# Optimization experiments

Measured on AMD Instinct MI355X. Metric: run time of the kernel, lower is better.

## Reference

```python
import jax, jax.numpy as jnp
import numpy as np

HIDDEN = 2048
NUM_V = 16
NUM_K = 8
HK = 128
HV = 128
KCONV = 4
KEY_DIM = NUM_K * HK      # 1024
VALUE_DIM = NUM_V * HV    # 2048
CONV_DIM = 2 * KEY_DIM + VALUE_DIM  # 4096
R = NUM_V // NUM_K        # 2
L2_EPS = 1e-6
NORM_EPS = 1e-6


def setup_inputs() -> dict:
    key = jax.random.key(0)
    ks = jax.random.split(key, 8)
    s = 0.02
    return {
        "hidden_states": jax.random.normal(ks[0], (1, 1024, HIDDEN), jnp.float32),
        "w_qkvz": jax.random.normal(ks[1], (2 * KEY_DIM + 2 * VALUE_DIM, HIDDEN), jnp.float32) * s,
        "w_ba": jax.random.normal(ks[2], (2 * NUM_V, HIDDEN), jnp.float32) * s,
        "conv_w": jax.random.normal(ks[3], (CONV_DIM, KCONV), jnp.float32) * s,
        "dt_bias": jnp.ones((NUM_V,), jnp.float32),
        "A_log": jnp.log(jax.random.uniform(ks[4], (NUM_V,), jnp.float32, 1e-3, 16.0)),
        "norm_weight": jnp.ones((HV,), jnp.float32),
        "w_out": jax.random.normal(ks[5], (HIDDEN, VALUE_DIM), jnp.float32) * s,
    }


def reference(hidden_states, w_qkvz, w_ba, conv_w, dt_bias, A_log, norm_weight, w_out):
    B, T, _ = hidden_states.shape
    # --- input projections ---
    qkvz = hidden_states @ w_qkvz.T                     # [B,T,2K+2V]
    ba = hidden_states @ w_ba.T                         # [B,T,2*Hv]
    # fix_query_key_value_ordering: group by k-head, layout [hk, hk, r*hv, r*hv]
    qkvz = qkvz.reshape(B, T, NUM_K, 2 * HK + 2 * R * HV)
    q, k, v, z = jnp.split(qkvz, [HK, 2 * HK, 2 * HK + R * HV], axis=3)
    v = v.reshape(B, T, NUM_V, HV)
    z = z.reshape(B, T, NUM_V, HV)
    ba = ba.reshape(B, T, NUM_K, 2 * R)
    b = ba[..., :R].reshape(B, T, NUM_V)
    a = ba[..., R:].reshape(B, T, NUM_V)
    # --- depthwise causal conv1d + silu over concatenated q,k,v ---
    mixed = jnp.concatenate(
        [q.reshape(B, T, KEY_DIM), k.reshape(B, T, KEY_DIM), v.reshape(B, T, VALUE_DIM)], axis=-1
    )
    xc = mixed.transpose(0, 2, 1)                       # [B,C,T]
    yc = jax.lax.conv_general_dilated(
        xc, conv_w[:, None, :], (1,), [(KCONV - 1, 0)],
        feature_group_count=CONV_DIM, dimension_numbers=("NCH", "OIH", "NCH"),
    )
    yc = jax.nn.silu(yc).transpose(0, 2, 1)             # [B,T,C]
    q, k, v = jnp.split(yc, [KEY_DIM, 2 * KEY_DIM], axis=-1)
    q = q.reshape(B, T, NUM_K, HK)
    k = k.reshape(B, T, NUM_K, HK)
    v = v.reshape(B, T, NUM_V, HV)
    # --- gates ---
    beta = jax.nn.sigmoid(b)                            # [B,T,Hv]
    g = -jnp.exp(A_log) * jax.nn.softplus(a + dt_bias)  # [B,T,Hv] (log decay, <=0)
    # GQA expansion of q,k to value heads
    q = jnp.repeat(q, R, axis=2)                        # [B,T,Hv,hk]
    k = jnp.repeat(k, R, axis=2)
    # l2 norm on q,k (use_qk_l2norm_in_kernel=True)
    q = q * jax.lax.rsqrt(jnp.sum(q * q, -1, keepdims=True) + L2_EPS)
    k = k * jax.lax.rsqrt(jnp.sum(k * k, -1, keepdims=True) + L2_EPS)
    scale = HK ** -0.5
    # --- gated delta rule recurrence ---
    def step(S, xs):
        qt, kt, vt, gt, bt = xs                          # per-timestep slices
        S = S * jnp.exp(gt)[..., None, None]             # decay state [B,Hv,hk,hv]
        kv = jnp.einsum("bhk,bhkv->bhv", kt, S)          # readout at k_t
        delta = (vt - kv) * bt[..., None]                # beta-gated delta
        S = S + jnp.einsum("bhk,bhv->bhkv", kt, delta)
        o = jnp.einsum("bhk,bhkv->bhv", qt * scale, S)
        return S, o

    S0 = jnp.zeros((B, NUM_V, HK, HV), hidden_states.dtype)
    xs = (
        q.transpose(1, 0, 2, 3), k.transpose(1, 0, 2, 3), v.transpose(1, 0, 2, 3),
        g.transpose(1, 0, 2), beta.transpose(1, 0, 2),
    )
    _, o = jax.lax.scan(step, S0, xs)                   # o: [T,B,Hv,hv]
    o = o.transpose(1, 0, 2, 3)                         # [B,T,Hv,hv]
    # --- gated RMSNorm (gate applied before normalization, Mamba2/Qwen3Next style) ---
    xf = o.astype(jnp.float32) * jax.nn.silu(z.astype(jnp.float32))
    var = jnp.mean(xf * xf, -1, keepdims=True)
    xn = xf * jax.lax.rsqrt(var + NORM_EPS) * norm_weight
    # --- output projection ---
    return xn.reshape(B, T, VALUE_DIM) @ w_out.T
```

## Files before the change

kernel.cpp:

```cpp
#include <hip/hip_runtime.h>
#include <math.h>

#define T_LEN   1024
#define HIDDEN  2048
#define QKVZ_N  6144
#define VAL_DIM 2048

typedef _Float16 half8 __attribute__((ext_vector_type(8)));
typedef _Float16 half4 __attribute__((ext_vector_type(4)));
typedef _Float16 half2t __attribute__((ext_vector_type(2)));
typedef float floatx4 __attribute__((ext_vector_type(4)));

__device__ __forceinline__ float sigmoidf_(float x) { return 1.f / (1.f + expf(-x)); }

__device__ __forceinline__ void gl_lds16(const _Float16* g, _Float16* l) {
    __builtin_amdgcn_global_load_lds(
        (const __attribute__((address_space(1))) void*)g,
        (__attribute__((address_space(3))) void*)l, 16, 0, 0);
}

__global__ __launch_bounds__(256) void cvt3(const float* __restrict__ s0, _Float16* __restrict__ d0, int n0,
                                            const float* __restrict__ s1, _Float16* __restrict__ d1, int n1,
                                            const float* __restrict__ s2, _Float16* __restrict__ d2, int n2) {
    int i = blockIdx.x * 256 + threadIdx.x;
    const float* s;
    _Float16* d;
    if (i < n0) { s = s0; d = d0; }
    else if (i < n0 + n1) { s = s1; d = d1; i -= n0; }
    else if (i < n0 + n1 + n2) { s = s2; d = d2; i -= n0 + n1; }
    else return;
    const float4 v = ((const float4*)s)[i];
    half4 h;
    h[0] = (_Float16)v.x; h[1] = (_Float16)v.y;
    h[2] = (_Float16)v.z; h[3] = (_Float16)v.w;
    *(half4*)&d[i * 4] = h;
}

template <typename OutT>
__global__ __launch_bounds__(256, 2) void gemm_h16(const _Float16* __restrict__ A,
                                                   const _Float16* __restrict__ W,
                                                   OutT* __restrict__ C,
                                                   int MB, int NB, int K) {
    const int N = NB * 128;
    const int l = blockIdx.x;
    const int x = l & 7;
    const int tt = l >> 3;
    const int mb = tt % MB;
    const int nb = x + 8 * (tt / MB);
    const int m0 = mb * 128, n0 = nb * 128;

    const int t = threadIdx.x;
    const int wave = t >> 6;
    const int lane = t & 63;
    const int wr = (wave >> 1) * 64;
    const int wc = (wave & 1) * 64;
    const int l15 = lane & 15;
    const int quad = lane >> 4;

    __shared__ __align__(16) _Float16 Ah[4096];
    __shared__ __align__(16) _Float16 Bh[4096];

    const int sr = lane >> 2;
    const int skq = lane & 3;

    floatx4 acc[4][4];
#pragma unroll
    for (int i = 0; i < 4; ++i)
#pragma unroll
        for (int j = 0; j < 4; ++j) acc[i][j] = 0;

    for (int k0 = 0; k0 < K; k0 += 32) {
        __syncthreads();
#pragma unroll
        for (int p = 0; p < 2; ++p) {
            const int r = p * 64 + wave * 16 + sr;
            const int kc = skq ^ (r & 3);
            const int lbase = (p * 256 + wave * 64) * 8;
            gl_lds16(A + (size_t)(m0 + r) * K + k0 + kc * 8, &Ah[lbase]);
            gl_lds16(W + (size_t)(n0 + r) * K + k0 + kc * 8, &Bh[lbase]);
        }
        __syncthreads();
        half8 af[4], bf[4];
#pragma unroll
        for (int mt = 0; mt < 4; ++mt) {
            const int m = wr + mt * 16 + l15;
            af[mt] = *(const half8*)&Ah[(m * 4 + (quad ^ (m & 3))) * 8];
        }
#pragma unroll
        for (int nt = 0; nt < 4; ++nt) {
            const int n = wc + nt * 16 + l15;
            bf[nt] = *(const half8*)&Bh[(n * 4 + (quad ^ (n & 3))) * 8];
        }
#pragma unroll
        for (int mt = 0; mt < 4; ++mt)
#pragma unroll
            for (int nt = 0; nt < 4; ++nt)
                acc[mt][nt] = __builtin_amdgcn_mfma_f32_16x16x32_f16(
                    af[mt], bf[nt], acc[mt][nt], 0, 0, 0);
    }
#pragma unroll
    for (int mt = 0; mt < 4; ++mt)
#pragma unroll
        for (int nt = 0; nt < 4; ++nt) {
            const int c = n0 + wc + nt * 16 + l15;
#pragma unroll
            for (int reg = 0; reg < 4; ++reg) {
                const int r = m0 + wr + mt * 16 + quad * 4 + reg;
                C[(size_t)r * N + c] = (OutT)acc[mt][nt][reg];
            }
        }
}

__global__ __launch_bounds__(256) void gemm_ba_gates(const float* __restrict__ A,
                                                     const float* __restrict__ W,
                                                     const float* __restrict__ dt_bias,
                                                     const float* __restrict__ A_log,
                                                     float* __restrict__ lgd,
                                                     float* __restrict__ bet) {
    const int m = blockIdx.x;
    const int tid = threadIdx.x;
    const int kl = tid & 31;
    const int ng = tid >> 5;
    const float* Arow = A + (size_t)m * 2048;
    __shared__ float sba[32];

    float4 a4[16];
#pragma unroll
    for (int j = 0; j < 16; ++j)
        a4[j] = *(const float4*)(Arow + j * 128 + kl * 4);

#pragma unroll
    for (int nn = 0; nn < 4; ++nn) {
        const int n = nn * 8 + ng;
        const float* Wrow = W + (size_t)n * 2048;
        float acc = 0.f;
#pragma unroll
        for (int j = 0; j < 16; ++j) {
            const float4 w4 = *(const float4*)(Wrow + j * 128 + kl * 4);
            acc = fmaf(a4[j].x, w4.x, acc);
            acc = fmaf(a4[j].y, w4.y, acc);
            acc = fmaf(a4[j].z, w4.z, acc);
            acc = fmaf(a4[j].w, w4.w, acc);
        }
        acc += __shfl_xor(acc, 1, 64);
        acc += __shfl_xor(acc, 2, 64);
        acc += __shfl_xor(acc, 4, 64);
        acc += __shfl_xor(acc, 8, 64);
        acc += __shfl_xor(acc, 16, 64);
        if (kl == 0) sba[n] = acc;
    }
    __syncthreads();
    if (tid < 16) {
        const int vh = tid, kh = vh >> 1, r = vh & 1;
        const float b = sba[kh * 4 + r];
        const float a = sba[kh * 4 + 2 + r];
        bet[m * 16 + vh] = 1.f / (1.f + expf(-b));
        const float xx = a + dt_bias[vh];
        const float sp = (xx > 0.f) ? (xx + log1pf(expf(-xx))) : log1pf(expf(xx));
        lgd[m * 16 + vh] = -expf(A_log[vh]) * sp;
    }
}

__global__ __launch_bounds__(256) void conv_silu(const _Float16* __restrict__ qkvz,
                                                 const float* __restrict__ conv_w,
                                                 _Float16* __restrict__ qc,
                                                 _Float16* __restrict__ kc,
                                                 _Float16* __restrict__ vc) {
    const int idx = blockIdx.x * 256 + threadIdx.x;
    const int t = idx >> 12;
    const int c = idx & 4095;
    int col;
    _Float16* dst;
    if (c < 1024) {
        col = ((c >> 7) * 768) + (c & 127);
        dst = qc + t * 1024 + c;
    } else if (c < 2048) {
        const int cc = c - 1024;
        col = ((cc >> 7) * 768) + 128 + (cc & 127);
        dst = kc + t * 1024 + cc;
    } else {
        const int cc = c - 2048;
        col = ((cc >> 8) * 768) + 256 + (cc & 255);
        dst = vc + t * 2048 + cc;
    }
    const float w0 = conv_w[c * 4 + 0];
    const float w1 = conv_w[c * 4 + 1];
    const float w2 = conv_w[c * 4 + 2];
    const float w3 = conv_w[c * 4 + 3];
    float acc = (float)qkvz[(size_t)t * QKVZ_N + col] * w3;
    if (t >= 1) acc = fmaf((float)qkvz[(size_t)(t - 1) * QKVZ_N + col], w2, acc);
    if (t >= 2) acc = fmaf((float)qkvz[(size_t)(t - 2) * QKVZ_N + col], w1, acc);
    if (t >= 3) acc = fmaf((float)qkvz[(size_t)(t - 3) * QKVZ_N + col], w0, acc);
    *dst = (_Float16)(acc * sigmoidf_(acc));
}

__global__ __launch_bounds__(64) void l2norm_qk(_Float16* __restrict__ qc,
                                                _Float16* __restrict__ kc) {
    const int b = blockIdx.x;
    const int t = b >> 4;
    const int hh = b & 15;
    _Float16* p;
    float extra;
    if (hh < 8) { p = qc + t * 1024 + hh * 128; extra = 0.08838834764831845f; }
    else        { p = kc + t * 1024 + (hh - 8) * 128; extra = 1.f; }
    const int j = threadIdx.x * 2;
    half2t x = *(const half2t*)(p + j);
    const float x0 = (float)x[0], x1 = (float)x[1];
    float ss = x0 * x0 + x1 * x1;
#pragma unroll
    for (int m = 1; m < 64; m <<= 1) ss += __shfl_xor(ss, m, 64);
    const float r = rsqrtf(ss + 1e-6f) * extra;
    half2t y; y[0] = (_Float16)(x0 * r); y[1] = (_Float16)(x1 * r);
    *(half2t*)(p + j) = y;
}

__global__ __launch_bounds__(256) void chunk_prep(
    const _Float16* __restrict__ qch, const _Float16* __restrict__ kch,
    const _Float16* __restrict__ vch, const float* __restrict__ lgd,
    const float* __restrict__ bet, _Float16* __restrict__ CH,
    float* __restrict__ gamC) {
    const int blk = blockIdx.x;
    const int c = blk >> 4, h = blk & 15, kh = h >> 1;
    const int c0 = c * 64;
    const int tid = threadIdx.x, lane = tid & 63, wave = tid >> 6;
    const int l15 = lane & 15, quad = lane >> 4;

    __shared__ __align__(16) _Float16 Ksh[8192];
    __shared__ __align__(16) _Float16 Qsh[8192];
    __shared__ float Amat[64 * 65];
    __shared__ float Gs[64], Bets[64], Gam[64];

    {
        const int t = tid >> 2, kc0 = (tid & 3) * 4;
        const size_t gb = (size_t)(c0 + t) * 1024 + kh * 128;
#pragma unroll
        for (int i = 0; i < 4; ++i) {
            const int kc = kc0 + i;
            half8 kv = *(const half8*)(kch + gb + kc * 8);
            half8 qv = *(const half8*)(qch + gb + kc * 8);
            const int chl = t * 16 + (kc ^ (t & 15));
            *(half8*)&Ksh[chl * 8] = kv;
            *(half8*)&Qsh[chl * 8] = qv;
        }
    }
    if (tid < 64) {
        float g = lgd[(size_t)(c0 + tid) * 16 + h];
#pragma unroll
        for (int off = 1; off < 64; off <<= 1) {
            float y = __shfl_up(g, off, 64);
            if (tid >= off) g += y;
        }
        Gs[tid] = g;
        Gam[tid] = expf(g);
        Bets[tid] = bet[(size_t)(c0 + tid) * 16 + h];
    }
    __syncthreads();

    _Float16* CHb = CH + (size_t)(c * 16 + h) * 36864;
    _Float16* Ug = CHb;
    _Float16* Wtg = CHb + 8192;
    _Float16* Khg = CHb + 16384;
    _Float16* Qgg = CHb + 24576;
    _Float16* Lg = CHb + 32768;

    {
        floatx4 accKK[4], accQK[4];
#pragma unroll
        for (int tt = 0; tt < 4; ++tt) { accKK[tt] = 0; accQK[tt] = 0; }
        half8 bfK[4];
#pragma unroll
        for (int ks = 0; ks < 4; ++ks) {
            const int i = wave * 16 + l15;
            const int kc = ks * 4 + quad;
            bfK[ks] = *(const half8*)&Ksh[(i * 16 + (kc ^ (i & 15))) * 8];
        }
#pragma unroll
        for (int tt = 0; tt < 4; ++tt) {
            const int t = tt * 16 + l15;
#pragma unroll
            for (int ks = 0; ks < 4; ++ks) {
                const int kc = ks * 4 + quad;
                const int chl = (t * 16 + (kc ^ (t & 15))) * 8;
                half8 afK = *(const half8*)&Ksh[chl];
                half8 afQ = *(const half8*)&Qsh[chl];
                accKK[tt] = __builtin_amdgcn_mfma_f32_16x16x32_f16(afK, bfK[ks], accKK[tt], 0, 0, 0);
                accQK[tt] = __builtin_amdgcn_mfma_f32_16x16x32_f16(afQ, bfK[ks], accQK[tt], 0, 0, 0);
            }
        }
        const int ii = wave * 16 + l15;
        const float Gi = Gs[ii];
#pragma unroll
        for (int tt = 0; tt < 4; ++tt)
#pragma unroll
            for (int r = 0; r < 4; ++r) {
                const int t = tt * 16 + quad * 4 + r;
                const float Gt = Gs[t];
                const float ratio = (ii <= t) ? expf(Gt - Gi) : 0.f;
                if (ii < t) Amat[t * 65 + ii] = Bets[t] * ratio * accKK[tt][r];
                Lg[t * 64 + ii] = (_Float16)((ii <= t) ? ratio * accQK[tt][r] : 0.f);
            }
    }
    __syncthreads();

    {
        const int j = tid;
        float x[64];
        if (j < 128) {
#pragma unroll
            for (int t = 0; t < 64; ++t)
                x[t] = Bets[t] * (float)vch[(size_t)(c0 + t) * 2048 + h * 128 + j];
        } else {
            const int k = j - 128;
#pragma unroll
            for (int t = 0; t < 64; ++t) {
                const int chl = t * 16 + ((k >> 3) ^ (t & 15));
                x[t] = Bets[t] * Gam[t] * (float)Ksh[chl * 8 + (k & 7)];
            }
        }
#pragma unroll
        for (int t = 1; t < 64; ++t) {
            float acc = 0.f;
#pragma unroll
            for (int i = 0; i < t; ++i) acc = fmaf(Amat[t * 65 + i], x[i], acc);
            x[t] -= acc;
        }
        if (j < 128) {
#pragma unroll
            for (int t = 0; t < 64; t += 4) {
                half4 w4;
                w4[0] = (_Float16)x[t]; w4[1] = (_Float16)x[t + 1];
                w4[2] = (_Float16)x[t + 2]; w4[3] = (_Float16)x[t + 3];
                *(half4*)&Wtg[j * 64 + t] = w4;
            }
        } else {
            const int k = j - 128;
#pragma unroll
            for (int t = 0; t < 64; ++t) Ug[t * 128 + k] = (_Float16)x[t];
        }
    }

    {
        const float g63 = Gs[63];
        const int k = tid >> 1, cb = (tid & 1) * 32;
#pragma unroll
        for (int cc = 0; cc < 32; cc += 4) {
            half4 o4;
#pragma unroll
            for (int u = 0; u < 4; ++u) {
                const int ci = cb + cc + u;
                const int chl = ci * 16 + ((k >> 3) ^ (ci & 15));
                o4[u] = (_Float16)(expf(g63 - Gs[ci]) * (float)Ksh[chl * 8 + (k & 7)]);
            }
            *(half4*)&Khg[k * 64 + cb + cc] = o4;
        }
        const int cq = tid >> 2, kb = (tid & 3) * 4;
        const float gam = Gam[cq];
#pragma unroll
        for (int kc = 0; kc < 4; ++kc) {
            const int kcc = kb + kc;
            half8 q8 = *(const half8*)&Qsh[(cq * 16 + (kcc ^ (cq & 15))) * 8];
            half8 s8;
#pragma unroll
            for (int u = 0; u < 8; ++u) s8[u] = (_Float16)(gam * (float)q8[u]);
            *(half8*)&Qgg[cq * 128 + kcc * 8] = s8;
        }
        if (tid == 0) gamC[c * 16 + h] = Gam[63];
    }
}

__global__ __launch_bounds__(256) void chunk_scan(const _Float16* __restrict__ CH,
                                                  const float* __restrict__ gamC,
                                                  float* __restrict__ o) {
    const int h = blockIdx.x >> 1, vs = blockIdx.x & 1;
    const int tid = threadIdx.x, lane = tid & 63, wave = tid >> 6;
    const int l15 = lane & 15, quad = lane >> 4;
    const int vrow = wave * 16 + l15;

    __shared__ __align__(16) _Float16 Sh[8192];
    __shared__ __align__(16) _Float16 Dt[4096];
    __shared__ __align__(16) _Float16 LUg[8704];
    __shared__ __align__(16) _Float16 LWt[4608];
    __shared__ __align__(16) _Float16 LKh[9216];
    __shared__ __align__(16) _Float16 LQg[8704];
    __shared__ __align__(16) _Float16 LLg[4608];

    floatx4 Sacc[8];
#pragma unroll
    for (int kt = 0; kt < 8; ++kt) Sacc[kt] = 0;
    for (int i = tid; i < 1024; i += 256) *(int4*)&Sh[i * 8] = make_int4(0, 0, 0, 0);
    __syncthreads();

    for (int c = 0; c < 16; ++c) {
        const _Float16* CHb = CH + (size_t)(c * 16 + h) * 36864;
        {
            const int4* src = (const int4*)CHb;
#pragma unroll
            for (int i = 0; i < 4; ++i) {
                const int idx = tid + i * 256;
                *(int4*)&LUg[((idx >> 4) * 17 + (idx & 15)) * 8] = src[idx];
            }
        }
        {
            const int4* src = (const int4*)(CHb + 8192 + vs * 4096);
#pragma unroll
            for (int i = 0; i < 2; ++i) {
                const int idx = tid + i * 256;
                *(int4*)&LWt[((idx >> 3) * 9 + (idx & 7)) * 8] = src[idx];
            }
        }
        {
            const int4* src = (const int4*)(CHb + 16384);
#pragma unroll
            for (int i = 0; i < 4; ++i) {
                const int idx = tid + i * 256;
                *(int4*)&LKh[((idx >> 3) * 9 + (idx & 7)) * 8] = src[idx];
            }
        }
        {
            const int4* src = (const int4*)(CHb + 24576);
#pragma unroll
            for (int i = 0; i < 4; ++i) {
                const int idx = tid + i * 256;
                *(int4*)&LQg[((idx >> 4) * 17 + (idx & 15)) * 8] = src[idx];
            }
        }
        {
            const int4* src = (const int4*)(CHb + 32768);
#pragma unroll
            for (int i = 0; i < 2; ++i) {
                const int idx = tid + i * 256;
                *(int4*)&LLg[((idx >> 3) * 9 + (idx & 7)) * 8] = src[idx];
            }
        }
        __syncthreads();

        half8 bs[4];
#pragma unroll
        for (int ks = 0; ks < 4; ++ks) {
            const int kc = ks * 4 + quad;
            bs[ks] = *(const half8*)&Sh[(vrow * 16 + (kc ^ (vrow & 15))) * 8];
        }
#pragma unroll
        for (int ct = 0; ct < 4; ++ct) {
            floatx4 xa = {0.f, 0.f, 0.f, 0.f};
#pragma unroll
            for (int ks = 0; ks < 4; ++ks) {
                half8 af = *(const half8*)&LUg[((ct * 16 + l15) * 17 + ks * 4 + quad) * 8];
                xa = __builtin_amdgcn_mfma_f32_16x16x32_f16(af, bs[ks], xa, 0, 0, 0);
            }
            half4 w4 = *(const half4*)&LWt[(vrow * 9 + ct * 2 + (quad >> 1)) * 8 + (quad & 1) * 4];
            half4 d4;
#pragma unroll
            for (int r = 0; r < 4; ++r) d4[r] = (_Float16)((float)w4[r] - xa[r]);
            const int cc = ct * 2 + (quad >> 1);
            *(half4*)&Dt[(vrow * 8 + (cc ^ (vrow & 7))) * 8 + (quad & 1) * 4] = d4;
        }
        half8 bd[2];
#pragma unroll
        for (int cs = 0; cs < 2; ++cs) {
            const int cc = cs * 4 + quad;
            bd[cs] = *(const half8*)&Dt[(vrow * 8 + (cc ^ (vrow & 7))) * 8];
        }
#pragma unroll
        for (int ct = 0; ct < 4; ++ct) {
            floatx4 oa = {0.f, 0.f, 0.f, 0.f};
#pragma unroll
            for (int ks = 0; ks < 4; ++ks) {
                half8 af = *(const half8*)&LQg[((ct * 16 + l15) * 17 + ks * 4 + quad) * 8];
                oa = __builtin_amdgcn_mfma_f32_16x16x32_f16(af, bs[ks], oa, 0, 0, 0);
            }
#pragma unroll
            for (int cs = 0; cs < 2; ++cs) {
                half8 af = *(const half8*)&LLg[((ct * 16 + l15) * 9 + cs * 4 + quad) * 8];
                oa = __builtin_amdgcn_mfma_f32_16x16x32_f16(af, bd[cs], oa, 0, 0, 0);
            }
            const int tg = c * 64 + ct * 16 + quad * 4;
            const int col = h * 128 + vs * 64 + vrow;
#pragma unroll
            for (int r = 0; r < 4; ++r) o[(size_t)(tg + r) * 2048 + col] = oa[r];
        }
        const float gC = gamC[c * 16 + h];
#pragma unroll
        for (int kt = 0; kt < 8; ++kt) {
#pragma unroll
            for (int r = 0; r < 4; ++r) Sacc[kt][r] *= gC;
#pragma unroll
            for (int cs = 0; cs < 2; ++cs) {
                half8 af = *(const half8*)&LKh[((kt * 16 + l15) * 9 + cs * 4 + quad) * 8];
                Sacc[kt] = __builtin_amdgcn_mfma_f32_16x16x32_f16(af, bd[cs], Sacc[kt], 0, 0, 0);
            }
        }
#pragma unroll
        for (int kt = 0; kt < 8; ++kt) {
            const int kc = kt * 2 + (quad >> 1);
            half4 s4;
#pragma unroll
            for (int r = 0; r < 4; ++r) s4[r] = (_Float16)Sacc[kt][r];
            *(half4*)&Sh[(vrow * 16 + (kc ^ (vrow & 15))) * 8 + (quad & 1) * 4] = s4;
        }
        __syncthreads();
    }
}

__global__ __launch_bounds__(64) void gated_norm(const float* __restrict__ o,
                                                 const _Float16* __restrict__ qkvz,
                                                 const float* __restrict__ nw,
                                                 _Float16* __restrict__ xn) {
    const int b = blockIdx.x;
    const int t = b >> 4;
    const int vh = b & 15;
    const int kh = vh >> 1;
    const int r = vh & 1;
    const float* op = o + (size_t)t * 2048 + vh * 128;
    const _Float16* zp = qkvz + (size_t)t * QKVZ_N + kh * 768 + 512 + r * 128;
    const int j = threadIdx.x * 2;
    const float2 ov = *(const float2*)(op + j);
    const half2t zv = *(const half2t*)(zp + j);
    const float z0 = (float)zv[0], z1 = (float)zv[1];
    const float f0 = ov.x * z0 / (1.f + expf(-z0));
    const float f1 = ov.y * z1 / (1.f + expf(-z1));
    float ss = f0 * f0 + f1 * f1;
#pragma unroll
    for (int m = 1; m < 64; m <<= 1) ss += __shfl_xor(ss, m, 64);
    const float rs = rsqrtf(ss * (1.f / 128.f) + 1e-6f);
    _Float16* xp = xn + (size_t)t * 2048 + vh * 128;
    half2t y;
    y[0] = (_Float16)(f0 * rs * nw[j]);
    y[1] = (_Float16)(f1 * rs * nw[j + 1]);
    *(half2t*)(xp + j) = y;
}

extern "C" void kernel_launch(void* const* d_in, const int* in_sizes, int n_in,
                              void* d_out, int out_size, void* d_ws, size_t ws_size,
                              hipStream_t stream) {
    const float* hidden  = (const float*)d_in[0];
    const float* w_qkvz  = (const float*)d_in[1];
    const float* w_ba    = (const float*)d_in[2];
    const float* conv_w  = (const float*)d_in[3];
    const float* dt_bias = (const float*)d_in[4];
    const float* A_log   = (const float*)d_in[5];
    const float* norm_w  = (const float*)d_in[6];
    const float* w_out   = (const float*)d_in[7];
    float* out = (float*)d_out;

    char* w = (char*)d_ws;
    _Float16*  qkvz_h = (_Float16*)(w);
    _Float16*  qch    = (_Float16*)(w + 12713984);
    _Float16*  kch    = (_Float16*)(w + 14811136);
    _Float16*  vch    = (_Float16*)(w + 16908288);
    float*     lgd    = (float*)(w + 21102592);
    float*     bet    = (float*)(w + 21168128);
    float*     gamC   = (float*)(w + 21233664);
    float*     o      = (float*)(w + 21237760);
    _Float16*  hid_h  = (_Float16*)(w + 21237760);
    _Float16*  wqk_h  = (_Float16*)(w + 29626368);
    _Float16*  CH     = (_Float16*)(w + 29626368);
    _Float16*  xn_h   = (_Float16*)(w + 29626368 + 18874368);
    _Float16*  wout_h = (_Float16*)(w + 54792192);

    const int n0 = HIDDEN * T_LEN / 4;
    const int n1 = QKVZ_N * HIDDEN / 4;
    const int n2 = VAL_DIM * HIDDEN / 4;
    cvt3<<<(n0 + n1 + n2 + 255) / 256, 256, 0, stream>>>(hidden, hid_h, n0,
                                                         w_qkvz, wqk_h, n1,
                                                         w_out, wout_h, n2);

    gemm_h16<_Float16><<<8 * 48, 256, 0, stream>>>(hid_h, wqk_h, qkvz_h, 8, 48, HIDDEN);
    gemm_ba_gates<<<T_LEN, 256, 0, stream>>>(hidden, w_ba, dt_bias, A_log, lgd, bet);
    conv_silu<<<(T_LEN * 4096) / 256, 256, 0, stream>>>(qkvz_h, conv_w, qch, kch, vch);
    l2norm_qk<<<T_LEN * 16, 64, 0, stream>>>(qch, kch);
    chunk_prep<<<256, 256, 0, stream>>>(qch, kch, vch, lgd, bet, CH, gamC);
    chunk_scan<<<32, 256, 0, stream>>>(CH, gamC, o);
    gated_norm<<<T_LEN * 16, 64, 0, stream>>>(o, qkvz_h, norm_w, xn_h);
    gemm_h16<float><<<8 * 16, 256, 0, stream>>>(xn_h, wout_h, out, 8, 16, HIDDEN);
}
```

Before: 316.0 us.

## Halve GEMM M-tile for more blocks and fuse conv-SiLU with L2 norm

The shared fp16 GEMM now uses 64x128 tiles instead of 128x128, which doubles the block count for both projections (768 and 256 blocks) so more CUs stay busy, and changes the LDS swizzle pattern. The separate conv_silu and l2norm_qk kernels are merged into a single kernel with one block per timestep. Each thread handles 8 channels with vector loads and reduces the per-head sum of squares using wave shuffles. This removes one launch and a global round trip for q/k, at the cost of lower per-block reuse in the GEMM.

```diff
diff --git a/kernel.cpp b/kernel.cpp
--- a/kernel.cpp
+++ b/kernel.cpp
@@ -47,59 +47,62 @@
     const int tt = l >> 3;
     const int mb = tt % MB;
     const int nb = x + 8 * (tt / MB);
-    const int m0 = mb * 128, n0 = nb * 128;
+    const int m0 = mb * 64, n0 = nb * 128;
 
     const int t = threadIdx.x;
     const int wave = t >> 6;
     const int lane = t & 63;
-    const int wr = (wave >> 1) * 64;
+    const int wr = (wave >> 1) * 32;
     const int wc = (wave & 1) * 64;
     const int l15 = lane & 15;
     const int quad = lane >> 4;
 
-    __shared__ __align__(16) _Float16 Ah[4096];
+    __shared__ __align__(16) _Float16 Ah[2048];
     __shared__ __align__(16) _Float16 Bh[4096];
 
     const int sr = lane >> 2;
     const int skq = lane & 3;
 
-    floatx4 acc[4][4];
-#pragma unroll
-    for (int i = 0; i < 4; ++i)
+    floatx4 acc[2][4];
+#pragma unroll
+    for (int i = 0; i < 2; ++i)
 #pragma unroll
         for (int j = 0; j < 4; ++j) acc[i][j] = 0;
 
     for (int k0 = 0; k0 < K; k0 += 32) {
         __syncthreads();
+        {
+            const int r = wave * 16 + sr;
+            const int kc = skq ^ ((r ^ (r >> 2)) & 3);
+            gl_lds16(A + (size_t)(m0 + r) * K + k0 + kc * 8, &Ah[wave * 512]);
+        }
 #pragma unroll
         for (int p = 0; p < 2; ++p) {
             const int r = p * 64 + wave * 16 + sr;
-            const int kc = skq ^ (r & 3);
-            const int lbase = (p * 256 + wave * 64) * 8;
-            gl_lds16(A + (size_t)(m0 + r) * K + k0 + kc * 8, &Ah[lbase]);
-            gl_lds16(W + (size_t)(n0 + r) * K + k0 + kc * 8, &Bh[lbase]);
+            const int kc = skq ^ ((r ^ (r >> 2)) & 3);
+            gl_lds16(W + (size_t)(n0 + r) * K + k0 + kc * 8, &Bh[p * 2048 + wave * 512]);
         }
         __syncthreads();
-        half8 af[4], bf[4];
-#pragma unroll
-        for (int mt = 0; mt < 4; ++mt) {
+        half8 af[2], bf[4];
+#pragma unroll
+        for (int mt = 0; mt < 2; ++mt) {
             const int m = wr + mt * 16 + l15;
-            af[mt] = *(const half8*)&Ah[(m * 4 + (quad ^ (m & 3))) * 8];
+            af[mt] = *(const half8*)&Ah[(m * 4 + (quad ^ ((m ^ (m >> 2)) & 3))) * 8];
         }
 #pragma unroll
         for (int nt = 0; nt < 4; ++nt) {
             const int n = wc + nt * 16 + l15;
-            bf[nt] = *(const half8*)&Bh[(n * 4 + (quad ^ (n & 3))) * 8];
-        }
-#pragma unroll
-        for (int mt = 0; mt < 4; ++mt)
+            bf[nt] = *(const half8*)&Bh[(n * 4 + (quad ^ ((n ^ (n >> 2)) & 3))) * 8];
+        }
+#pragma unroll
+        for (int mt = 0; mt < 2; ++mt)
 #pragma unroll
             for (int nt = 0; nt < 4; ++nt)
                 acc[mt][nt] = __builtin_amdgcn_mfma_f32_16x16x32_f16(
                     af[mt], bf[nt], acc[mt][nt], 0, 0, 0);
     }
 #pragma unroll
-    for (int mt = 0; mt < 4; ++mt)
+    for (int mt = 0; mt < 2; ++mt)
 #pragma unroll
         for (int nt = 0; nt < 4; ++nt) {
             const int c = n0 + wc + nt * 16 + l15;
@@ -161,57 +164,67 @@
     }
 }
 
-__global__ __launch_bounds__(256) void conv_silu(const _Float16* __restrict__ qkvz,
-                                                 const float* __restrict__ conv_w,
-                                                 _Float16* __restrict__ qc,
-                                                 _Float16* __restrict__ kc,
-                                                 _Float16* __restrict__ vc) {
-    const int idx = blockIdx.x * 256 + threadIdx.x;
-    const int t = idx >> 12;
-    const int c = idx & 4095;
+__global__ __launch_bounds__(512) void conv_silu_l2(const _Float16* __restrict__ qkvz,
+                                                    const float* __restrict__ conv_w,
+                                                    _Float16* __restrict__ qc,
+                                                    _Float16* __restrict__ kc,
+                                                    _Float16* __restrict__ vc) {
+    const int t = blockIdx.x;
+    const int c = threadIdx.x * 8;
     int col;
     _Float16* dst;
+    bool isqk;
+    float extra = 1.f;
     if (c < 1024) {
         col = ((c >> 7) * 768) + (c & 127);
         dst = qc + t * 1024 + c;
+        isqk = true;
+        extra = 0.08838834764831845f;
     } else if (c < 2048) {
         const int cc = c - 1024;
         col = ((cc >> 7) * 768) + 128 + (cc & 127);
         dst = kc + t * 1024 + cc;
+        isqk = true;
     } else {
         const int cc = c - 2048;
         col = ((cc >> 8) * 768) + 256 + (cc & 255);
-        dst = vc + t * 2048 + cc;
-    }
-    const float w0 = conv_w[c * 4 + 0];
-    const float w1 = conv_w[c * 4 + 1];
-    const float w2 = conv_w[c * 4 + 2];
-    const float w3 = conv_w[c * 4 + 3];
-    float acc = (float)qkvz[(size_t)t * QKVZ_N + col] * w3;
-    if (t >= 1) acc = fmaf((float)qkvz[(size_t)(t - 1) * QKVZ_N + col], w2, acc);
-    if (t >= 2) acc = fmaf((float)qkvz[(size_t)(t - 2) * QKVZ_N + col], w1, acc);
-    if (t >= 3) acc = fmaf((float)qkvz[(size_t)(t - 3) * QKVZ_N + col], w0, acc);
-    *dst = (_Float16)(acc * sigmoidf_(acc));
-}
-
-__global__ __launch_bounds__(64) void l2norm_qk(_Float16* __restrict__ qc,
-                                                _Float16* __restrict__ kc) {
-    const int b = blockIdx.x;
-    const int t = b >> 4;
-    const int hh = b & 15;
-    _Float16* p;
-    float extra;
-    if (hh < 8) { p = qc + t * 1024 + hh * 128; extra = 0.08838834764831845f; }
-    else        { p = kc + t * 1024 + (hh - 8) * 128; extra = 1.f; }
-    const int j = threadIdx.x * 2;
-    half2t x = *(const half2t*)(p + j);
-    const float x0 = (float)x[0], x1 = (float)x[1];
-    float ss = x0 * x0 + x1 * x1;
-#pragma unroll
-    for (int m = 1; m < 64; m <<= 1) ss += __shfl_xor(ss, m, 64);
-    const float r = rsqrtf(ss + 1e-6f) * extra;
-    half2t y; y[0] = (_Float16)(x0 * r); y[1] = (_Float16)(x1 * r);
-    *(half2t*)(p + j) = y;
+        dst = vc + (size_t)t * 2048 + cc;
+        isqk = false;
+    }
+    const size_t gb = (size_t)t * QKVZ_N + col;
+    const half8 x3 = *(const half8*)(qkvz + gb);
+    half8 x2, x1, x0;
+    if (t >= 1) x2 = *(const half8*)(qkvz + gb - QKVZ_N);
+    if (t >= 2) x1 = *(const half8*)(qkvz + gb - 2 * (size_t)QKVZ_N);
+    if (t >= 3) x0 = *(const half8*)(qkvz + gb - 3 * (size_t)QKVZ_N);
+
+    float y[8];
+    float ss = 0.f;
+#pragma unroll
+    for (int u = 0; u < 8; ++u) {
+        const float4 wv = *(const float4*)(conv_w + (c + u) * 4);
+        float acc = (float)x3[u] * wv.w;
+        if (t >= 1) acc = fmaf((float)x2[u], wv.z, acc);
+        if (t >= 2) acc = fmaf((float)x1[u], wv.y, acc);
+        if (t >= 3) acc = fmaf((float)x0[u], wv.x, acc);
+        acc = acc * (1.f / (1.f + expf(-acc)));
+        y[u] = acc;
+        ss = fmaf(acc, acc, ss);
+    }
+    half8 ov;
+    if (isqk) {
+        ss += __shfl_xor(ss, 1, 64);
+        ss += __shfl_xor(ss, 2, 64);
+        ss += __shfl_xor(ss, 4, 64);
+        ss += __shfl_xor(ss, 8, 64);
+        const float r = rsqrtf(ss + 1e-6f) * extra;
+#pragma unroll
+        for (int u = 0; u < 8; ++u) ov[u] = (_Float16)(y[u] * r);
+    } else {
+#pragma unroll
+        for (int u = 0; u < 8; ++u) ov[u] = (_Float16)y[u];
+    }
+    *(half8*)dst = ov;
 }
 
 __global__ __launch_bounds__(256) void chunk_prep(
@@ -565,12 +578,11 @@
                                                          w_qkvz, wqk_h, n1,
                                                          w_out, wout_h, n2);
 
-    gemm_h16<_Float16><<<8 * 48, 256, 0, stream>>>(hid_h, wqk_h, qkvz_h, 8, 48, HIDDEN);
+    gemm_h16<_Float16><<<16 * 48, 256, 0, stream>>>(hid_h, wqk_h, qkvz_h, 16, 48, HIDDEN);
     gemm_ba_gates<<<T_LEN, 256, 0, stream>>>(hidden, w_ba, dt_bias, A_log, lgd, bet);
-    conv_silu<<<(T_LEN * 4096) / 256, 256, 0, stream>>>(qkvz_h, conv_w, qch, kch, vch);
-    l2norm_qk<<<T_LEN * 16, 64, 0, stream>>>(qch, kch);
+    conv_silu_l2<<<T_LEN, 512, 0, stream>>>(qkvz_h, conv_w, qch, kch, vch);
     chunk_prep<<<256, 256, 0, stream>>>(qch, kch, vch, lgd, bet, CH, gamC);
     chunk_scan<<<32, 256, 0, stream>>>(CH, gamC, o);
     gated_norm<<<T_LEN * 16, 64, 0, stream>>>(o, qkvz_h, norm_w, xn_h);
-    gemm_h16<float><<<8 * 16, 256, 0, stream>>>(xn_h, wout_h, out, 8, 16, HIDDEN);
-}
+    gemm_h16<float><<<16 * 16, 256, 0, stream>>>(xn_h, wout_h, out, 16, 16, HIDDEN);
+}
```

Result: no change. 313.4 us (-0.8%).
